# Performance work log

Measured on AMD Instinct MI355X. Metric: run time of the kernel, lower is better.

Reference implementation:

```python
import jax, jax.numpy as jnp
import numpy as np

MULTI_INFER_NUM = 8
D_EMBED = 128
N_LAYERS = 2
T, B = 2048, 32


def setup_inputs() -> dict:
    key = jax.random.key(0)
    k1, k2, k3, k4 = jax.random.split(key, 4)
    positions = jax.random.randint(k1, (T, B), 0, 16, dtype=jnp.int64)
    outputs = jax.random.normal(k2, (T, B, D_EMBED), dtype=jnp.float32)
    # 4 LinearTransferFeatures per layer (self_forget, logit, logit_forget, out_forget)
    Ws = jax.random.normal(k3, (N_LAYERS, 4, MULTI_INFER_NUM + 1, D_EMBED, D_EMBED), dtype=jnp.float32) * 0.05
    bs = jax.random.normal(k4, (N_LAYERS, 4, MULTI_INFER_NUM + 1, D_EMBED), dtype=jnp.float32) * 0.05
    return {"positions": positions, "outputs": outputs, "Ws": Ws, "bs": bs}


def _linear(x, onehot, W, b):
    # x: [t,b,d]; onehot: [t,b,e]; W: [e,d,f]; b: [e,d]
    # Equivalent to gathering W[r_pos] ([t,b,d,f]) then einsum('ibde,ibd->ibe'),
    # but computed as per-expert GEMMs + one-hot combine (grouped-GEMM form).
    y_all = jnp.einsum('tbd,edf->tbef', x, W)      # per-expert outputs
    y = jnp.einsum('tbef,tbe->tbf', y_all, onehot)  # select token's expert
    return y + jnp.einsum('tbe,ed->tbd', onehot, b)


def reference(positions, outputs, Ws, bs):
    m = Ws.shape[2] - 1  # multi_infer_num
    r_pos = jnp.where(positions < m, positions, m)
    onehot = jax.nn.one_hot(r_pos, m + 1, dtype=outputs.dtype)
    x = outputs
    for l in range(Ws.shape[0]):
        self_forget = _linear(x, onehot, Ws[l, 0], bs[l, 0])
        logit = _linear(x, onehot, Ws[l, 1], bs[l, 1])
        logit_forget = _linear(x, onehot, Ws[l, 2], bs[l, 2])
        out_forget = _linear(x, onehot, Ws[l, 3], bs[l, 3])
        new_res = x * jax.nn.sigmoid(self_forget) + jnp.tanh(logit) * jax.nn.sigmoid(logit_forget)
        x = jnp.tanh(new_res) * jax.nn.sigmoid(out_forget)
    return x
```

## Files before the change

### kernel.cpp

```cpp
#include <hip/hip_runtime.h>
#include <hip/hip_fp16.h>
#include <stdint.h>

#define TOKENS 65536
#define D      128
#define NEXP   9
#define MT     32
#define MAXTILES (TOKENS / MT + NEXP)
#define NHB    256

typedef _Float16 f16;
typedef _Float16 f16x8  __attribute__((ext_vector_type(8)));
typedef float    f32x4  __attribute__((ext_vector_type(4)));
typedef uint32_t u32;

#define WI_TOKOFF  32
#define WI_TILEOFF 48
#define WI_HIST    128
#define WI_PERM    4736
#define WS_WF_OFF  ((4736 + TOKENS) * 4)

#define LOG2E  1.44269504f

__global__ void k_prep(const float* __restrict__ Ws, const int* __restrict__ pos,
                       int* __restrict__ wsI, f16* __restrict__ Wf) {
  const int tid = threadIdx.x;
  if (blockIdx.x < 288) {
    const int mat = blockIdx.x >> 2;
    const int q   = blockIdx.x & 3;
    const float* src = Ws + (size_t)mat * (D * D);
    f16* dst = Wf + (size_t)mat * (D * D);
#pragma unroll
    for (int p = 0; p < 2; ++p) {
      int cc = q * 512 + p * 256 + tid;
      int ln = cc & 63;
      int kb = (cc >> 6) & 3;
      int c  = cc >> 8;
      int quad = ln >> 4, n = ln & 15;
      int f  = c * 16 + n;
      int d0 = kb * 32 + quad * 8;
      f16x8 w;
#pragma unroll
      for (int i = 0; i < 8; ++i) w[i] = (f16)src[(d0 + i) * D + f];
      *(f16x8*)(dst + cc * 8) = w;
    }
  } else {
    const int b = blockIdx.x - 288;
    __shared__ int h[NEXP];
    if (tid < NEXP) h[tid] = 0;
    __syncthreads();
    int e = pos[b * 256 + tid]; e = e < 8 ? e : 8;
    atomicAdd(&h[e], 1);
    __syncthreads();
    if (tid < NEXP) wsI[WI_HIST + b * NEXP + tid] = h[tid];
  }
}

__global__ void k_scan_assign(const int* __restrict__ pos, int* __restrict__ wsI) {
  const int tid = threadIdx.x, b = blockIdx.x;
  const int lane = tid & 63, w = tid >> 6;
  __shared__ int wsum[4];
  __shared__ int totS[NEXP];
  __shared__ int relB[NEXP];
  __shared__ int baseS[NEXP];
  __shared__ int waveCnt[4][NEXP];
  __shared__ int waveBase[4][NEXP];

  int myE = pos[b * 256 + tid]; myE = myE < 8 ? myE : 8;

  int myh[NEXP];
#pragma unroll
  for (int e = 0; e < NEXP; ++e) myh[e] = wsI[WI_HIST + tid * NEXP + e];

  for (int e = 0; e < NEXP; ++e) {
    int v = myh[e];
    int x = v;
#pragma unroll
    for (int off = 1; off < 64; off <<= 1) {
      int y = __shfl_up(x, off);
      if (lane >= off) x += y;
    }
    if (lane == 63) wsum[w] = x;
    __syncthreads();
    int add = 0;
    for (int w2 = 0; w2 < w; ++w2) add += wsum[w2];
    int incl = x + add;
    if (tid == b)   relB[e] = incl - v;
    if (tid == 255) totS[e] = incl;
    __syncthreads();
  }
  if (tid == 0) {
    int tok = 0, tile = 0;
    if (b == 0) { wsI[WI_TOKOFF] = 0; wsI[WI_TILEOFF] = 0; }
    for (int e = 0; e < NEXP; ++e) {
      baseS[e] = tok + relB[e];
      int cnt = totS[e];
      tok += cnt; tile += (cnt + MT - 1) / MT;
      if (b == 0) { wsI[WI_TOKOFF + e + 1] = tok; wsI[WI_TILEOFF + e + 1] = tile; }
    }
  }
  int myRank = 0;
#pragma unroll
  for (int ee = 0; ee < NEXP; ++ee) {
    unsigned long long m = __ballot(myE == ee);
    if (myE == ee) myRank = __popcll(m & ((1ull << lane) - 1ull));
    if (lane == 0) waveCnt[w][ee] = __popcll(m);
  }
  __syncthreads();
  if (tid < NEXP) {
    int s = 0;
#pragma unroll
    for (int w2 = 0; w2 < 4; ++w2) { waveBase[w2][tid] = s; s += waveCnt[w2][tid]; }
  }
  __syncthreads();
  wsI[WI_PERM + baseS[myE] + waveBase[w][myE] + myRank] = b * 256 + tid;
}

__launch_bounds__(256, 3)
__global__ void k_main(const float* __restrict__ xin, const float* __restrict__ bsPtr,
                       const int* __restrict__ wsI, const f16* __restrict__ Wf,
                       float* __restrict__ outPtr) {
  __shared__ __attribute__((aligned(16))) f16 Ash[MT][136];
  __shared__ float Bsh[8][D];
  __shared__ int s_tok[MT];

  const int tid = threadIdx.x;
  const int bid = blockIdx.x;
  const int ntiles = wsI[WI_TILEOFF + NEXP];
  if (bid >= ntiles) return;

  int e = 0, tileOffE = 0;
#pragma unroll
  for (int ee = 0; ee < NEXP; ee++) {
    int to = wsI[WI_TILEOFF + ee];
    if (to <= bid) { e = ee; tileOffE = to; }
  }
  const int tokStart = wsI[WI_TOKOFF + e] + (bid - tileOffE) * MT;
  const int tokEnd   = wsI[WI_TOKOFF + e + 1];
  const int rowsValid = min(MT, tokEnd - tokStart);

  const int lane = tid & 63;
  const int n    = lane & 15;
  const int quad = lane >> 4;
  const int cBase = (tid >> 6) * 2;
  const int vlane = lane * 8;
  const f16* We = Wf + (size_t)e * 16384;

  f16x8 bb[16];
#define LOADB(LL, CC)                                                          \
  do {                                                                         \
    const f16* _base = We + (size_t)(LL) * 4 * 147456 + (CC) * 2048 + vlane;   \
    _Pragma("unroll")                                                          \
    for (int _j = 0; _j < 4; ++_j)                                             \
      _Pragma("unroll")                                                        \
      for (int _kb = 0; _kb < 4; ++_kb)                                        \
        bb[_j * 4 + _kb] = *(const f16x8*)(_base + _j * 147456 + _kb * 512);   \
  } while (0)

#define LOAD_AF()                                                              \
  do {                                                                         \
    _Pragma("unroll")                                                          \
    for (int _kb = 0; _kb < 4; ++_kb) {                                        \
      aF0[_kb] = *(const f16x8*)&Ash[n][_kb * 32 + quad * 8];                  \
      aF1[_kb] = *(const f16x8*)&Ash[16 + n][_kb * 32 + quad * 8];             \
    }                                                                          \
  } while (0)

  LOADB(0, cBase);

  {
    int mat = tid >> 5, d = (tid & 31) * 4;
    float4 bv = *(const float4*)(bsPtr + (size_t)(mat * NEXP + e) * D + d);
    *(float4*)&Bsh[mat][d] = bv;
  }

  {
    int m = tid >> 3, h = tid & 7;
    bool valid = (m < rowsValid);
    int tok = 0;
    if (valid) tok = wsI[WI_PERM + tokStart + m];
    if (h == 0) s_tok[m] = valid ? tok : -1;
    const float4* src = (const float4*)(xin + (size_t)tok * D + h * 16);
    f16* drow = &Ash[m][h * 16];
#pragma unroll
    for (int i = 0; i < 2; i++) {
      float4 a = make_float4(0.f, 0.f, 0.f, 0.f), b2 = a;
      if (valid) { a = src[2 * i]; b2 = src[2 * i + 1]; }
      f16x8 wv;
      wv[0] = (f16)a.x;  wv[1] = (f16)a.y;  wv[2] = (f16)a.z;  wv[3] = (f16)a.w;
      wv[4] = (f16)b2.x; wv[5] = (f16)b2.y; wv[6] = (f16)b2.z; wv[7] = (f16)b2.w;
      *(f16x8*)&drow[i * 8] = wv;
    }
  }
  __syncthreads();

  f16x8 aF0[4], aF1[4];
  LOAD_AF();
  __syncthreads();

  const int f0 = cBase * 16 + n;

#pragma unroll 1
  for (int l = 0; l < 2; l++) {
#pragma unroll
    for (int ci = 0; ci < 2; ci++) {
      const int f = f0 + ci * 16;

      f32x4 acc[4][2];
      __builtin_amdgcn_s_setprio(1);
#pragma unroll
      for (int j = 0; j < 4; ++j) {
        f32x4 x0 = {0.f, 0.f, 0.f, 0.f}, x1 = {0.f, 0.f, 0.f, 0.f};
#pragma unroll
        for (int kb = 0; kb < 4; ++kb) {
          x0 = __builtin_amdgcn_mfma_f32_16x16x32_f16(aF0[kb], bb[j * 4 + kb], x0, 0, 0, 0);
          x1 = __builtin_amdgcn_mfma_f32_16x16x32_f16(aF1[kb], bb[j * 4 + kb], x1, 0, 0, 0);
        }
        acc[j][0] = x0; acc[j][1] = x1;
      }
      __builtin_amdgcn_s_setprio(0);

      if (ci == 0)      LOADB(l, cBase + 1);
      else if (l == 0)  LOADB(1, cBase);

      float bv0 = Bsh[l * 4 + 0][f];
      float bv1 = Bsh[l * 4 + 1][f];
      float bv2 = Bsh[l * 4 + 2][f];
      float bv3 = Bsh[l * 4 + 3][f];
      float xv[2][4];
#pragma unroll
      for (int s = 0; s < 2; s++)
#pragma unroll
        for (int r = 0; r < 4; r++)
          xv[s][r] = (float)Ash[s * 16 + quad * 4 + r][f];

#pragma unroll
      for (int s = 0; s < 2; s++) {
#pragma unroll
        for (int r = 0; r < 4; r++) {
          int m = s * 16 + quad * 4 + r;
          float sf = acc[0][s][r] + bv0;
          float lg = acc[1][s][r] + bv1;
          float lf = acc[2][s][r] + bv2;
          float of = acc[3][s][r] + bv3;
          float Ea = __builtin_amdgcn_exp2f(-LOG2E * sf);
          float Eb = __builtin_amdgcn_exp2f((2.0f * LOG2E) * lg);
          float Ec = __builtin_amdgcn_exp2f(-LOG2E * lf);
          float d1 = 1.0f + Ea, d2 = Eb + 1.0f, d3 = 1.0f + Ec;
          float p23 = d2 * d3;
          float nr = (xv[s][r] * p23 + (Eb - 1.0f) * d1) *
                     __builtin_amdgcn_rcpf(d1 * p23);
          float Ed = __builtin_amdgcn_exp2f((2.0f * LOG2E) * nr);
          float Ee = __builtin_amdgcn_exp2f(-LOG2E * of);
          float xn = (Ed - 1.0f) * __builtin_amdgcn_rcpf((Ed + 1.0f) * (1.0f + Ee));
          if (l == 0) {
            Ash[m][f] = (f16)xn;
          } else {
            int tok = s_tok[m];
            if (tok >= 0) outPtr[(size_t)tok * D + f] = xn;
          }
        }
      }
    }
    if (l == 0) {
      __syncthreads();
      LOAD_AF();
    }
  }
#undef LOADB
#undef LOAD_AF
}

extern "C" void kernel_launch(void* const* d_in, const int* in_sizes, int n_in,
                              void* d_out, int out_size, void* d_ws, size_t ws_size,
                              hipStream_t stream) {
  const int*   pos = (const int*)d_in[0];
  const float* x   = (const float*)d_in[1];
  const float* Ws  = (const float*)d_in[2];
  const float* bs  = (const float*)d_in[3];
  float* out = (float*)d_out;
  int* wsI = (int*)d_ws;
  f16* Wf = (f16*)((char*)d_ws + WS_WF_OFF);

  k_prep       <<<544, 256, 0, stream>>>(Ws, pos, wsI, Wf);
  k_scan_assign<<<NHB, 256, 0, stream>>>(pos, wsI);
  k_main       <<<MAXTILES, 256, 0, stream>>>(x, bs, wsI, Wf, out);
}
```

Baseline: 142.3 us.

## Double-buffer weight fragments per gate to cut registers and raise occupancy

Replaces the 16-register-vector weight preload with two 4-vector ping-pong buffers, prefetching the next gate's weights while MFMAs run on the current one. Biases are loaded directly into registers and used as the accumulator initial value, which removes the shared-memory bias table and the separate bias adds. The stage loop is fully unrolled, the setprio hints are dropped, and launch bounds go from 3 to 4 blocks per SIMD. The aim is lower VGPR pressure and higher occupancy, at the cost of less prefetch distance, so load latency may be exposed between gates.

```diff
diff --git a/kernel.cpp b/kernel.cpp
--- a/kernel.cpp
+++ b/kernel.cpp
@@ -116,12 +116,11 @@
   wsI[WI_PERM + baseS[myE] + waveBase[w][myE] + myRank] = b * 256 + tid;
 }
 
-__launch_bounds__(256, 3)
+__launch_bounds__(256, 4)
 __global__ void k_main(const float* __restrict__ xin, const float* __restrict__ bsPtr,
                        const int* __restrict__ wsI, const f16* __restrict__ Wf,
                        float* __restrict__ outPtr) {
   __shared__ __attribute__((aligned(16))) f16 Ash[MT][136];
-  __shared__ float Bsh[8][D];
   __shared__ int s_tok[MT];
 
   const int tid = threadIdx.x;
@@ -145,16 +144,19 @@
   const int cBase = (tid >> 6) * 2;
   const int vlane = lane * 8;
   const f16* We = Wf + (size_t)e * 16384;
-
-  f16x8 bb[16];
-#define LOADB(LL, CC)                                                          \
-  do {                                                                         \
-    const f16* _base = We + (size_t)(LL) * 4 * 147456 + (CC) * 2048 + vlane;   \
-    _Pragma("unroll")                                                          \
-    for (int _j = 0; _j < 4; ++_j)                                             \
+  const int f0 = cBase * 16 + n;
+
+  f16x8 aF0[4], aF1[4];
+  f16x8 b0[4], b1[4];
+
+#define PFB(BUF, LL, CC, JJ)                                                   \
+  do {                                                                         \
+    if ((LL) < 2) {                                                            \
+      const f16* _p = We + ((LL) * 4 + (JJ)) * 147456 + (CC) * 2048 + vlane;   \
       _Pragma("unroll")                                                        \
       for (int _kb = 0; _kb < 4; ++_kb)                                        \
-        bb[_j * 4 + _kb] = *(const f16x8*)(_base + _j * 147456 + _kb * 512);   \
+        BUF[_kb] = *(const f16x8*)(_p + _kb * 512);                            \
+    }                                                                          \
   } while (0)
 
 #define LOAD_AF()                                                              \
@@ -166,13 +168,28 @@
     }                                                                          \
   } while (0)
 
-  LOADB(0, cBase);
-
-  {
-    int mat = tid >> 5, d = (tid & 31) * 4;
-    float4 bv = *(const float4*)(bsPtr + (size_t)(mat * NEXP + e) * D + d);
-    *(float4*)&Bsh[mat][d] = bv;
-  }
+#define MFMA2(G, BUF, BV)                                                      \
+  do {                                                                         \
+    f32x4 _x = {(BV), (BV), (BV), (BV)};                                       \
+    f32x4 _y = _x;                                                             \
+    _Pragma("unroll")                                                          \
+    for (int _kb = 0; _kb < 4; ++_kb) {                                        \
+      _x = __builtin_amdgcn_mfma_f32_16x16x32_f16(aF0[_kb], BUF[_kb], _x, 0, 0, 0); \
+      _y = __builtin_amdgcn_mfma_f32_16x16x32_f16(aF1[_kb], BUF[_kb], _y, 0, 0, 0); \
+    }                                                                          \
+    acc[G][0] = _x; acc[G][1] = _y;                                            \
+  } while (0)
+
+  PFB(b0, 0, cBase, 0);
+
+  float bias[2][2][4];
+#pragma unroll
+  for (int l = 0; l < 2; ++l)
+#pragma unroll
+    for (int ci = 0; ci < 2; ++ci)
+#pragma unroll
+      for (int j = 0; j < 4; ++j)
+        bias[l][ci][j] = bsPtr[((l * 4 + j) * NEXP + e) * D + f0 + ci * 16];
 
   {
     int m = tid >> 3, h = tid & 7;
@@ -193,82 +210,69 @@
     }
   }
   __syncthreads();
-
-  f16x8 aF0[4], aF1[4];
   LOAD_AF();
   __syncthreads();
 
-  const int f0 = cBase * 16 + n;
-
-#pragma unroll 1
-  for (int l = 0; l < 2; l++) {
-#pragma unroll
-    for (int ci = 0; ci < 2; ci++) {
-      const int f = f0 + ci * 16;
-
-      f32x4 acc[4][2];
-      __builtin_amdgcn_s_setprio(1);
-#pragma unroll
-      for (int j = 0; j < 4; ++j) {
-        f32x4 x0 = {0.f, 0.f, 0.f, 0.f}, x1 = {0.f, 0.f, 0.f, 0.f};
-#pragma unroll
-        for (int kb = 0; kb < 4; ++kb) {
-          x0 = __builtin_amdgcn_mfma_f32_16x16x32_f16(aF0[kb], bb[j * 4 + kb], x0, 0, 0, 0);
-          x1 = __builtin_amdgcn_mfma_f32_16x16x32_f16(aF1[kb], bb[j * 4 + kb], x1, 0, 0, 0);
-        }
-        acc[j][0] = x0; acc[j][1] = x1;
-      }
-      __builtin_amdgcn_s_setprio(0);
-
-      if (ci == 0)      LOADB(l, cBase + 1);
-      else if (l == 0)  LOADB(1, cBase);
-
-      float bv0 = Bsh[l * 4 + 0][f];
-      float bv1 = Bsh[l * 4 + 1][f];
-      float bv2 = Bsh[l * 4 + 2][f];
-      float bv3 = Bsh[l * 4 + 3][f];
-      float xv[2][4];
-#pragma unroll
-      for (int s = 0; s < 2; s++)
-#pragma unroll
-        for (int r = 0; r < 4; r++)
-          xv[s][r] = (float)Ash[s * 16 + quad * 4 + r][f];
-
-#pragma unroll
-      for (int s = 0; s < 2; s++) {
-#pragma unroll
-        for (int r = 0; r < 4; r++) {
-          int m = s * 16 + quad * 4 + r;
-          float sf = acc[0][s][r] + bv0;
-          float lg = acc[1][s][r] + bv1;
-          float lf = acc[2][s][r] + bv2;
-          float of = acc[3][s][r] + bv3;
-          float Ea = __builtin_amdgcn_exp2f(-LOG2E * sf);
-          float Eb = __builtin_amdgcn_exp2f((2.0f * LOG2E) * lg);
-          float Ec = __builtin_amdgcn_exp2f(-LOG2E * lf);
-          float d1 = 1.0f + Ea, d2 = Eb + 1.0f, d3 = 1.0f + Ec;
-          float p23 = d2 * d3;
-          float nr = (xv[s][r] * p23 + (Eb - 1.0f) * d1) *
-                     __builtin_amdgcn_rcpf(d1 * p23);
-          float Ed = __builtin_amdgcn_exp2f((2.0f * LOG2E) * nr);
-          float Ee = __builtin_amdgcn_exp2f(-LOG2E * of);
-          float xn = (Ed - 1.0f) * __builtin_amdgcn_rcpf((Ed + 1.0f) * (1.0f + Ee));
-          if (l == 0) {
-            Ash[m][f] = (f16)xn;
-          } else {
-            int tok = s_tok[m];
-            if (tok >= 0) outPtr[(size_t)tok * D + f] = xn;
-          }
-        }
-      }
-    }
-    if (l == 0) {
-      __syncthreads();
-      LOAD_AF();
-    }
-  }
-#undef LOADB
+#define STAGE(L, CI, NL, NC)                                                   \
+  do {                                                                         \
+    const int cc = cBase + (CI);                                               \
+    const int f = f0 + (CI) * 16;                                              \
+    f32x4 acc[4][2];                                                           \
+    PFB(b1, L, cc, 1);  MFMA2(0, b0, bias[L][CI][0]);                          \
+    PFB(b0, L, cc, 2);  MFMA2(1, b1, bias[L][CI][1]);                          \
+    PFB(b1, L, cc, 3);  MFMA2(2, b0, bias[L][CI][2]);                          \
+    PFB(b0, NL, NC, 0); MFMA2(3, b1, bias[L][CI][3]);                          \
+    \
+    float xv[2][4];                                                            \
+    _Pragma("unroll")                                                          \
+    for (int s = 0; s < 2; s++)                                                \
+      _Pragma("unroll")                                                        \
+      for (int r = 0; r < 4; r++)                                              \
+        xv[s][r] = (float)Ash[s * 16 + quad * 4 + r][f];                       \
+    _Pragma("unroll")                                                          \
+    for (int s = 0; s < 2; s++) {                                              \
+      _Pragma("unroll")                                                        \
+      for (int r = 0; r < 4; r++) {                                            \
+        int m = s * 16 + quad * 4 + r;              \
+        float sf = acc[0][s][r];                    \
+        float lg = acc[1][s][r];                                               \
+        float lf = acc[2][s][r];                                               \
+        float of = acc[3][s][r];                                               \
+         \
+         \
+         \
+        float Ea = __builtin_amdgcn_exp2f(-LOG2E * sf);                        \
+        float Eb = __builtin_amdgcn_exp2f((2.0f * LOG2E) * lg);                \
+        float Ec = __builtin_amdgcn_exp2f(-LOG2E * lf);                        \
+        float d1 = 1.0f + Ea, d2 = Eb + 1.0f, d3 = 1.0f + Ec;                  \
+        float p23 = d2 * d3;                                                   \
+        float nr = (xv[s][r] * p23 + (d2 - 2.0f) * d1) *                       \
+                   __builtin_amdgcn_rcpf(d1 * p23);                            \
+                        \
+        float Ed = __builtin_amdgcn_exp2f((2.0f * LOG2E) * nr);                \
+        float Ee = __builtin_amdgcn_exp2f(-LOG2E * of);                        \
+        float xn = (Ed - 1.0f) * __builtin_amdgcn_rcpf((Ed + 1.0f) * (1.0f + Ee)); \
+        if ((L) == 0) {                                                        \
+          Ash[m][f] = (f16)xn;                   \
+        } else {                                                               \
+          int tok = s_tok[m];                                                  \
+          if (tok >= 0) outPtr[(size_t)tok * D + f] = xn;                      \
+        }                                                                      \
+      }                                                                        \
+    }                                                                          \
+  } while (0)
+
+  STAGE(0, 0, 0, cBase + 1);
+  STAGE(0, 1, 1, cBase);
+  __syncthreads();
+  LOAD_AF();
+  STAGE(1, 0, 1, cBase + 1);
+  STAGE(1, 1, 2, 0);
+
+#undef STAGE
+#undef MFMA2
 #undef LOAD_AF
+#undef PFB
 }
 
 extern "C" void kernel_launch(void* const* d_in, const int* in_sizes, int n_in,
```

New measurement: 129.5 us. 9.0% less time.
